# Kernel tuning notes

Measured on AMD Instinct MI355X. Metric: run time of the kernel, lower is better.

## Reference

```python
import jax, jax.numpy as jnp
import numpy as np

B, C, F, D = 128, 16, 128, 512


def setup_inputs() -> dict:
    key = jax.random.key(0)
    k1, k2 = jax.random.split(key)
    return {
        "c_feats": jax.random.normal(k1, (B, C, D), dtype=jnp.float32),
        "f_feats": jax.random.normal(k2, (B, F, D), dtype=jnp.float32),
    }


def _dtw_path_masks(S):
    """S: [P, c, f] per-pair similarity. Returns [P, c, f] 0/1 max-path masks.

    DP: D[i,j] = max(D[i-1,j], D[i,j-1], D[i-1,j-1]) + S[i-1,j-1], D[0,0]=0,
    borders -inf. Tie-break priority (up, left, diag) matches Python max().
    Row recurrence is vectorized: D[i,j] = Csum[j] + cummax_k<=j(A[k]-Csum[k-1])
    where A[k]=max(D[i-1,k], D[i-1,k-1]) (wavefront-free row-parallel form).
    """
    P_, c, f = S.shape
    NEG = -jnp.inf

    init = jnp.concatenate([jnp.zeros((P_, 1), S.dtype),
                            jnp.full((P_, f), NEG, S.dtype)], axis=1)  # D[0, 0..f]

    def row_step(prev, dt_row):
        # prev: [P, f+1] = D[i-1, 0..f]; dt_row: [P, f] = S[i-1, :]
        A = jnp.maximum(prev[:, 1:], prev[:, :-1])                  # max(D[i-1,j], D[i-1,j-1])
        Ccum = jnp.cumsum(dt_row, axis=1)
        Cm1 = jnp.concatenate([jnp.zeros((P_, 1), dt_row.dtype), Ccum[:, :-1]], axis=1)
        row = Ccum + jax.lax.cummax(A - Cm1, axis=1)                # D[i, 1..f]
        new_prev = jnp.concatenate([jnp.full((P_, 1), NEG, dt_row.dtype), row], axis=1)
        return new_prev, new_prev

    _, rows = jax.lax.scan(row_step, init, jnp.moveaxis(S, 1, 0))   # [c, P, f+1]
    Dm = jnp.moveaxis(jnp.concatenate([init[None], rows], axis=0), 1, 0)  # [P, c+1, f+1]

    # Predecessor choice per cell; argmax picks first max -> priority up,left,diag
    up = Dm[:, :-1, 1:]
    left = Dm[:, 1:, :-1]
    diag = Dm[:, :-1, :-1]
    mv = jnp.argmax(jnp.stack([up, left, diag], axis=-1), axis=-1).astype(jnp.int32)
    mv = jnp.pad(mv, ((0, 0), (1, 0), (1, 0)))                      # [P, c+1, f+1]

    pidx = jnp.arange(P_)

    def bt_step(carry, _):
        mask, i, j = carry
        active = (i > 0) | (j > 0)
        mask = mask.at[pidx, i - 1, j - 1].add(jnp.where(active, 1.0, 0.0).astype(mask.dtype))
        m = mv[pidx, i, j]
        di = jnp.where(m == 1, 0, 1)   # left keeps i
        dj = jnp.where(m == 0, 0, 1)   # up keeps j
        i = jnp.where(active, i - di, i)
        j = jnp.where(active, j - dj, j)
        return (mask, i, j), None

    mask0 = jnp.zeros((P_, c, f), jnp.float32)
    i0 = jnp.full((P_,), c, jnp.int32)
    j0 = jnp.full((P_,), f, jnp.int32)
    (mask, _, _), _ = jax.lax.scan(bt_step, (mask0, i0, j0), None, length=c + f)
    return mask


def reference(c_feats, f_feats):
    b, c, d = c_feats.shape
    f = f_feats.shape[1]
    xn = c_feats / jnp.linalg.norm(c_feats, axis=-1, keepdims=True)
    yn = f_feats / jnp.linalg.norm(f_feats, axis=-1, keepdims=True)
    # Source quirk: y row j is normalized only once outer index i reaches it
    # (y[i-1] bug), so S[i,j] uses normalized y[j] iff j <= i, raw y[j] otherwise.
    Sn = jnp.einsum('mcd,nfd->mncf', xn, yn)
    Sr = jnp.einsum('mcd,nfd->mncf', xn, f_feats)
    tri = jnp.arange(f)[None, :] <= jnp.arange(c)[:, None]          # [c, f]: j <= i
    S = jnp.where(tri, Sn, Sr).reshape(b * b, c, f)
    return _dtw_path_masks(S).reshape(b, b, c, f)
```

## Files before the change

kernel.cpp:

```cpp
#include <hip/hip_runtime.h>
#include <stdint.h>

#define M_TOT 2048
#define N_TOT 16384
#define K_TOT 512

typedef _Float16 f16x8 __attribute__((ext_vector_type(8)));
typedef float f32x4 __attribute__((ext_vector_type(4)));
typedef float f32x16 __attribute__((ext_vector_type(16)));

#define AS1 __attribute__((address_space(1)))
#define AS3 __attribute__((address_space(3)))

__device__ __forceinline__ void ld_lds16(const void* g, void* l) {
    __builtin_amdgcn_global_load_lds((const AS1 void*)g, (AS3 void*)l, 16, 0, 0);
}

__device__ __forceinline__ void split4(float x0, float x1, float x2, float x3,
                                       uint2* hs, uint2* ls) {
    union U { _Float16 h[4]; uint2 u; } H, L;
    _Float16 h0 = (_Float16)x0; H.h[0] = h0; L.h[0] = (_Float16)(x0 - (float)h0);
    _Float16 h1 = (_Float16)x1; H.h[1] = h1; L.h[1] = (_Float16)(x1 - (float)h1);
    _Float16 h2 = (_Float16)x2; H.h[2] = h2; L.h[2] = (_Float16)(x2 - (float)h2);
    _Float16 h3 = (_Float16)x3; H.h[3] = h3; L.h[3] = (_Float16)(x3 - (float)h3);
    *hs = H.u; *ls = L.u;
}

__global__ __launch_bounds__(256) void norm_split_kernel(
    const float* __restrict__ c_feats, const float* __restrict__ f_feats,
    _Float16* __restrict__ Ah, _Float16* __restrict__ Al,
    _Float16* __restrict__ Bh, _Float16* __restrict__ Bl,
    float* __restrict__ normf)
{
    int wave = blockIdx.x * 4 + (threadIdx.x >> 6);
    int lane = threadIdx.x & 63;
    if (wave < 2048) {
        const float* row = c_feats + (size_t)wave * K_TOT;
        float4 v0 = ((const float4*)row)[lane];
        float4 v1 = ((const float4*)row)[lane + 64];
        double ss = (double)v0.x * v0.x + (double)v0.y * v0.y +
                    (double)v0.z * v0.z + (double)v0.w * v0.w +
                    (double)v1.x * v1.x + (double)v1.y * v1.y +
                    (double)v1.z * v1.z + (double)v1.w * v1.w;
        #pragma unroll
        for (int off = 32; off; off >>= 1) ss += __shfl_down(ss, off);
        double tot = __shfl(ss, 0);
        float nrm = sqrtf((float)tot);
        float a0 = v0.x / nrm, a1 = v0.y / nrm, a2 = v0.z / nrm, a3 = v0.w / nrm;
        float b0 = v1.x / nrm, b1 = v1.y / nrm, b2 = v1.z / nrm, b3 = v1.w / nrm;
        uint2 h, l;
        split4(a0, a1, a2, a3, &h, &l);
        ((uint2*)(Ah + (size_t)wave * K_TOT))[lane] = h;
        ((uint2*)(Al + (size_t)wave * K_TOT))[lane] = l;
        split4(b0, b1, b2, b3, &h, &l);
        ((uint2*)(Ah + (size_t)wave * K_TOT))[lane + 64] = h;
        ((uint2*)(Al + (size_t)wave * K_TOT))[lane + 64] = l;
    } else if (wave < 18432) {
        int fr = wave - 2048;
        const float* row = f_feats + (size_t)fr * K_TOT;
        float4 v0 = ((const float4*)row)[lane];
        float4 v1 = ((const float4*)row)[lane + 64];
        double ss = (double)v0.x * v0.x + (double)v0.y * v0.y +
                    (double)v0.z * v0.z + (double)v0.w * v0.w +
                    (double)v1.x * v1.x + (double)v1.y * v1.y +
                    (double)v1.z * v1.z + (double)v1.w * v1.w;
        #pragma unroll
        for (int off = 32; off; off >>= 1) ss += __shfl_down(ss, off);
        if (lane == 0) normf[fr] = sqrtf((float)ss);
        uint2 h, l;
        split4(v0.x, v0.y, v0.z, v0.w, &h, &l);
        ((uint2*)(Bh + (size_t)fr * K_TOT))[lane] = h;
        ((uint2*)(Bl + (size_t)fr * K_TOT))[lane] = l;
        split4(v1.x, v1.y, v1.z, v1.w, &h, &l);
        ((uint2*)(Bh + (size_t)fr * K_TOT))[lane + 64] = h;
        ((uint2*)(Bl + (size_t)fr * K_TOT))[lane + 64] = l;
    }
}

__global__ __launch_bounds__(256, 2) void mfma_gemm_kernel(
    const _Float16* __restrict__ Ah, const _Float16* __restrict__ Al,
    const _Float16* __restrict__ Bh, const _Float16* __restrict__ Bl,
    const float* __restrict__ normf,
    float* __restrict__ out)
{
    __shared__ _Float16 sAh[128 * 32];
    __shared__ _Float16 sAl[128 * 32];
    __shared__ _Float16 sBh[128 * 32];
    __shared__ _Float16 sBl[128 * 32];

    const int t = threadIdx.x;
    const int w = t >> 6, lane = t & 63;
    const int gm0 = blockIdx.y * 128, gn0 = blockIdx.x * 128;
    const int wm = (w & 1) * 64, wn = (w >> 1) * 64;
    const int m32 = lane & 31;
    const int kql0 = lane >> 5;

    f32x16 acc[2][2] = {};
    const int l0 = w * 128 + lane;

    for (int k0 = 0; k0 < K_TOT; k0 += 32) {
        #pragma unroll
        for (int c = 0; c < 2; ++c) {
            int l = l0 + c * 64;
            int lrow = l >> 2, kq = l & 3;
            int kqs = kq ^ ((lrow >> 1) & 3);
            size_t goffA = (size_t)(gm0 + lrow) * K_TOT + k0 + kqs * 8;
            size_t goffB = (size_t)(gn0 + lrow) * K_TOT + k0 + kqs * 8;
            ld_lds16(Ah + goffA, sAh + (size_t)l * 8);
            ld_lds16(Al + goffA, sAl + (size_t)l * 8);
            ld_lds16(Bh + goffB, sBh + (size_t)l * 8);
            ld_lds16(Bl + goffB, sBl + (size_t)l * 8);
        }
        __syncthreads();

        #pragma unroll
        for (int kh = 0; kh < 2; ++kh) {
            f16x8 fah[2], fal[2], fbh[2], fbl[2];
            #pragma unroll
            for (int x = 0; x < 2; ++x) {
                int arr = wm + x * 32 + m32;
                int brr = wn + x * 32 + m32;
                int kqa = (kh * 2 + kql0) ^ ((arr >> 1) & 3);
                int kqb = (kh * 2 + kql0) ^ ((brr >> 1) & 3);
                int ar = arr * 32 + kqa * 8;
                int br = brr * 32 + kqb * 8;
                fah[x] = *(const f16x8*)(sAh + ar);
                fal[x] = *(const f16x8*)(sAl + ar);
                fbh[x] = *(const f16x8*)(sBh + br);
                fbl[x] = *(const f16x8*)(sBl + br);
            }
            #pragma unroll
            for (int mi = 0; mi < 2; ++mi)
                #pragma unroll
                for (int ni = 0; ni < 2; ++ni) {
                    acc[mi][ni] = __builtin_amdgcn_mfma_f32_32x32x16_f16(fah[mi], fbl[ni], acc[mi][ni], 0, 0, 0);
                    acc[mi][ni] = __builtin_amdgcn_mfma_f32_32x32x16_f16(fal[mi], fbh[ni], acc[mi][ni], 0, 0, 0);
                    acc[mi][ni] = __builtin_amdgcn_mfma_f32_32x32x16_f16(fah[mi], fbh[ni], acc[mi][ni], 0, 0, 0);
                }
        }
        __syncthreads();
    }

    const int nn = blockIdx.x;
    const int rq = 4 * (lane >> 5);
    #pragma unroll
    for (int ni = 0; ni < 2; ++ni) {
        int col = wn + ni * 32 + m32;
        bool cn = (col < 16);
        float nf = cn ? normf[gn0 + col] : 1.f;
        #pragma unroll
        for (int mi = 0; mi < 2; ++mi) {
            #pragma unroll
            for (int reg = 0; reg < 16; ++reg) {
                int r = wm + mi * 32 + (reg & 3) + 8 * (reg >> 2) + rq;
                int gm = gm0 + r;
                int mm = gm >> 4, ii = gm & 15;
                float v = acc[mi][ni][reg];
                if (cn && col <= ii) v /= nf;
                out[(((size_t)mm * 128 + nn) * 16 + ii) * 128 + col] = v;
            }
        }
    }
}

__global__ __launch_bounds__(256) void dtw_kernel(float* __restrict__ buf)
{
    __shared__ uint32_t mvw[4][4][132];
    __shared__ int bounds[4][4][16];

    const int lane = threadIdx.x & 63;
    const int w = threadIdx.x >> 6;
    const int q = lane >> 4, r = lane & 15;
    const int pbase = blockIdx.x * 16 + w * 4;
    const int p = pbase + q;
    float* tile = buf + (size_t)p * 2048;
    const float4* row4 = (const float4*)(tile + r * 128);
    uint32_t* mvq = &mvw[w][q][0];

    const double NEG = -1e300;
    double Dp = NEG, Dp2 = NEG;
    float4 cur4 = {0, 0, 0, 0};
    float4 nxt4 = row4[0];
    float4 nx2  = row4[1];
    float4 nx3  = row4[2];
    uint32_t mvbuf = 0;

#define DTW_STEP(T, BOUNDARY)                                                   \
    {                                                                           \
        int j = (T) - r;                                                        \
        bool act = (j >= 0) & (j < 128);                                        \
        if (act & ((j & 3) == 0)) {                                             \
            cur4 = nxt4; nxt4 = nx2; nx2 = nx3;                                 \
            if (j + 12 < 128) nx3 = row4[(j >> 2) + 3];                         \
        }                                                                       \
        int e = j & 3;                                                          \
        float sv = (e == 0) ? cur4.x : (e == 1) ? cur4.y                        \
                 : (e == 2) ? cur4.z : cur4.w;                                  \
        double up = __shfl_up(Dp, 1);                                           \
        double dg = __shfl_up(Dp2, 1);                                          \
        double lf = Dp;                                                         \
        if (r == 0) up = NEG;                                                   \
        if (BOUNDARY) {                                                         \
            if (j == 0) {                                                       \
                lf = NEG;                                                       \
                dg = (r == 0) ? 0.0 : NEG;                                      \
            } else if (r == 0) {                                                \
                dg = NEG;                                                       \
            }                                                                   \
        } else {                                                                \
            if (r == 0) dg = NEG;                                               \
        }                                                                       \
        int m = (up >= lf && up >= dg) ? 0 : ((lf >= dg) ? 1 : 2);              \
        double Dc = fmax(up, fmax(lf, dg)) + (double)sv;                        \
        if (act) {                                                              \
            mvbuf |= (uint32_t)m << (2 * (j & 15));                             \
            if ((j & 15) == 15) {                                               \
                mvq[r * 8 + (j >> 4)] = mvbuf;                                  \
                mvbuf = 0;                                                      \
            }                                                                   \
        }                                                                       \
        Dp2 = Dp;                                                               \
        Dp = Dc;                                                                \
    }

    for (int t = 0; t < 16; ++t) DTW_STEP(t, true)
    for (int t = 16; t < 143; ++t) DTW_STEP(t, false)
#undef DTW_STEP

    __syncthreads();

    if (r == 0) {
        int i = 16, jj = 128, hic = 127;
        for (int it = 0; it < 160; ++it) {
            if (i <= 0) break;
            uint32_t word = mvq[(i - 1) * 8 + ((jj - 1) >> 4)];
            int m = (int)((word >> (2 * ((jj - 1) & 15))) & 3u);
            if (m == 1) { --jj; continue; }
            bounds[w][q][i - 1] = (jj - 1) | (hic << 8);
            if (m == 2) --jj;
            --i;
            hic = jj - 1;
        }
    }
    __syncthreads();

    #pragma unroll 4
    for (int it = 0; it < 32; ++it) {
        int flat = it * 64 + lane;
        int q2 = flat >> 9;
        int rem = flat & 511;
        int ii = rem >> 5;
        int c4 = rem & 31;
        int b = bounds[w][q2][ii];
        int lo = b & 0xff, hi = (b >> 8) & 0xff;
        int j0 = c4 * 4;
        float4 v;
        v.x = (j0 + 0 >= lo && j0 + 0 <= hi) ? 1.f : 0.f;
        v.y = (j0 + 1 >= lo && j0 + 1 <= hi) ? 1.f : 0.f;
        v.z = (j0 + 2 >= lo && j0 + 2 <= hi) ? 1.f : 0.f;
        v.w = (j0 + 3 >= lo && j0 + 3 <= hi) ? 1.f : 0.f;
        float* tb = buf + (size_t)(pbase + q2) * 2048;
        *(float4*)(tb + ii * 128 + j0) = v;
    }
}

extern "C" void kernel_launch(void* const* d_in, const int* in_sizes, int n_in,
                              void* d_out, int out_size, void* d_ws, size_t ws_size,
                              hipStream_t stream)
{
    const float* c_feats = (const float*)d_in[0];
    const float* f_feats = (const float*)d_in[1];
    float* out = (float*)d_out;

    _Float16* Ah = (_Float16*)d_ws;
    _Float16* Al = Ah + (size_t)M_TOT * K_TOT;
    _Float16* Bh = Al + (size_t)M_TOT * K_TOT;
    _Float16* Bl = Bh + (size_t)N_TOT * K_TOT;
    float* normf = (float*)(Bl + (size_t)N_TOT * K_TOT);

    norm_split_kernel<<<4608, 256, 0, stream>>>(c_feats, f_feats, Ah, Al, Bh, Bl, normf);
    dim3 g(N_TOT / 128, M_TOT / 128);
    mfma_gemm_kernel<<<g, 256, 0, stream>>>(Ah, Al, Bh, Bl, normf, out);
    dtw_kernel<<<1024, 256, 0, stream>>>(out);
}
```

Baseline: 368.9 us.

## Stage DTW similarity tiles through double-buffered LDS and drop the second shuffle

```diff
diff --git a/kernel.cpp b/kernel.cpp
--- a/kernel.cpp
+++ b/kernel.cpp
@@ -163,8 +163,12 @@
     }
 }
 
+#define DQS 552
+#define DBUFS 2208
+
 __global__ __launch_bounds__(256) void dtw_kernel(float* __restrict__ buf)
 {
+    __shared__ float swin[4][2 * DBUFS];
     __shared__ uint32_t mvw[4][4][132];
     __shared__ int bounds[4][4][16];
 
@@ -172,68 +176,101 @@
     const int w = threadIdx.x >> 6;
     const int q = lane >> 4, r = lane & 15;
     const int pbase = blockIdx.x * 16 + w * 4;
-    const int p = pbase + q;
-    float* tile = buf + (size_t)p * 2048;
-    const float4* row4 = (const float4*)(tile + r * 128);
+    const float4* gbase = (const float4*)(buf + (size_t)pbase * 2048);
+    float* sw = swin[w];
     uint32_t* mvq = &mvw[w][q][0];
 
+    int gidx[8], lidx[8];
+    #pragma unroll
+    for (int i = 0; i < 8; ++i) {
+        int f4 = i * 64 + lane;
+        gidx[i] = (f4 >> 7) * 512 + ((f4 >> 3) & 15) * 32 + (f4 & 7);
+        lidx[i] = (f4 >> 7) * DQS + ((f4 >> 3) & 15) * 34 + (f4 & 7) * 4;
+    }
+
+    float4 ga[8], gb[8];
+    #pragma unroll
+    for (int i = 0; i < 8; ++i) ga[i] = gbase[gidx[i]];
+    #pragma unroll
+    for (int i = 0; i < 8; ++i) gb[i] = gbase[gidx[i] + 8];
+    #pragma unroll
+    for (int i = 0; i < 8; ++i) {
+        *(float2*)(sw + lidx[i])     = make_float2(ga[i].x, ga[i].y);
+        *(float2*)(sw + lidx[i] + 2) = make_float2(ga[i].z, ga[i].w);
+    }
+    #pragma unroll
+    for (int i = 0; i < 8; ++i) {
+        *(float2*)(sw + DBUFS + lidx[i])     = make_float2(gb[i].x, gb[i].y);
+        *(float2*)(sw + DBUFS + lidx[i] + 2) = make_float2(gb[i].z, gb[i].w);
+    }
+    #pragma unroll
+    for (int i = 0; i < 8; ++i) ga[i] = gbase[gidx[i] + 16];
+    __syncthreads();
+
     const double NEG = -1e300;
-    double Dp = NEG, Dp2 = NEG;
-    float4 cur4 = {0, 0, 0, 0};
-    float4 nxt4 = row4[0];
-    float4 nx2  = row4[1];
-    float4 nx3  = row4[2];
+    double Dp = NEG, rawprev = NEG;
     uint32_t mvbuf = 0;
-
-#define DTW_STEP(T, BOUNDARY)                                                   \
+    int j = -r;
+    const int sb = q * DQS + r * 34;
+
+#define DTW_STEP(BOUNDARY)                                                      \
     {                                                                           \
-        int j = (T) - r;                                                        \
-        bool act = (j >= 0) & (j < 128);                                        \
-        if (act & ((j & 3) == 0)) {                                             \
-            cur4 = nxt4; nxt4 = nx2; nx2 = nx3;                                 \
-            if (j + 12 < 128) nx3 = row4[(j >> 2) + 3];                         \
-        }                                                                       \
-        int e = j & 3;                                                          \
-        float sv = (e == 0) ? cur4.x : (e == 1) ? cur4.y                        \
-                 : (e == 2) ? cur4.z : cur4.w;                                  \
-        double up = __shfl_up(Dp, 1);                                           \
-        double dg = __shfl_up(Dp2, 1);                                          \
+        double upr = __shfl_up(Dp, 1);                                          \
+        double dg = rawprev;                                                    \
+        rawprev = upr;                                                          \
+        double up = (r == 0) ? NEG : upr;                                       \
         double lf = Dp;                                                         \
-        if (r == 0) up = NEG;                                                   \
         if (BOUNDARY) {                                                         \
-            if (j == 0) {                                                       \
-                lf = NEG;                                                       \
-                dg = (r == 0) ? 0.0 : NEG;                                      \
-            } else if (r == 0) {                                                \
-                dg = NEG;                                                       \
-            }                                                                   \
+            if (j == 0) { lf = NEG; dg = (r == 0) ? 0.0 : NEG; }                \
+            else if (r == 0) dg = NEG;                                          \
         } else {                                                                \
             if (r == 0) dg = NEG;                                               \
         }                                                                       \
+        float sv = sw[((j & 32) ? DBUFS : 0) + sb + (j & 31)];                  \
         int m = (up >= lf && up >= dg) ? 0 : ((lf >= dg) ? 1 : 2);              \
         double Dc = fmax(up, fmax(lf, dg)) + (double)sv;                        \
-        if (act) {                                                              \
+        if ((unsigned)j < 128u) {                                               \
             mvbuf |= (uint32_t)m << (2 * (j & 15));                             \
-            if ((j & 15) == 15) {                                               \
-                mvq[r * 8 + (j >> 4)] = mvbuf;                                  \
-                mvbuf = 0;                                                      \
-            }                                                                   \
+            if ((j & 15) == 15) { mvq[r * 8 + (j >> 4)] = mvbuf; mvbuf = 0; }   \
         }                                                                       \
-        Dp2 = Dp;                                                               \
         Dp = Dc;                                                                \
-    }
-
-    for (int t = 0; t < 16; ++t) DTW_STEP(t, true)
-    for (int t = 16; t < 143; ++t) DTW_STEP(t, false)
+        ++j;                                                                    \
+    }
+
+    for (int t = 0; t < 16; ++t) DTW_STEP(true)
+    for (int t = 16; t < 48; ++t) DTW_STEP(false)
+
+    #pragma unroll
+    for (int i = 0; i < 8; ++i) {
+        *(float2*)(sw + lidx[i])     = make_float2(ga[i].x, ga[i].y);
+        *(float2*)(sw + lidx[i] + 2) = make_float2(ga[i].z, ga[i].w);
+    }
+    #pragma unroll
+    for (int i = 0; i < 8; ++i) gb[i] = gbase[gidx[i] + 24];
+    __syncthreads();
+
+    for (int t = 48; t < 80; ++t) DTW_STEP(false)
+
+    #pragma unroll
+    for (int i = 0; i < 8; ++i) {
+        *(float2*)(sw + DBUFS + lidx[i])     = make_float2(gb[i].x, gb[i].y);
+        *(float2*)(sw + DBUFS + lidx[i] + 2) = make_float2(gb[i].z, gb[i].w);
+    }
+    __syncthreads();
+
+    for (int t = 80; t < 143; ++t) DTW_STEP(false)
 #undef DTW_STEP
 
     __syncthreads();
 
     if (r == 0) {
         int i = 16, jj = 128, hic = 127;
+        int cidx = -1;
+        uint32_t word = 0;
         for (int it = 0; it < 160; ++it) {
             if (i <= 0) break;
-            uint32_t word = mvq[(i - 1) * 8 + ((jj - 1) >> 4)];
+            int idx = (i - 1) * 8 + ((jj - 1) >> 4);
+            if (idx != cidx) { word = mvq[idx]; cidx = idx; }
             int m = (int)((word >> (2 * ((jj - 1) & 15))) & 3u);
             if (m == 1) { --jj; continue; }
             bounds[w][q][i - 1] = (jj - 1) | (hic << 8);
```

New measurement: 357.6 us. 1.03x faster.
